# Optimization experiments

Hardware: AMD Instinct MI355X
Metric: run time of the kernel (lower is better)

Reference implementation:

```python
import jax, jax.numpy as jnp
import numpy as np

H = 32  # hidden size, fixed by the source module


def setup_inputs() -> dict:
    key = jax.random.key(0)
    ks = jax.random.split(key, 11)
    B, T = 1024, 999
    s = 0.1  # weight init scale
    return {
        "input": jax.random.normal(ks[0], (B, T), jnp.float32),
        "W_ih1": jax.random.normal(ks[1], (4 * H, 1), jnp.float32) * s,
        "W_hh1": jax.random.normal(ks[2], (4 * H, H), jnp.float32) * s,
        "b_ih1": jax.random.normal(ks[3], (4 * H,), jnp.float32) * s,
        "b_hh1": jax.random.normal(ks[4], (4 * H,), jnp.float32) * s,
        "W_ih2": jax.random.normal(ks[5], (4 * H, H), jnp.float32) * s,
        "W_hh2": jax.random.normal(ks[6], (4 * H, H), jnp.float32) * s,
        "b_ih2": jax.random.normal(ks[7], (4 * H,), jnp.float32) * s,
        "b_hh2": jax.random.normal(ks[8], (4 * H,), jnp.float32) * s,
        "W_lin": jax.random.normal(ks[9], (1, H), jnp.float32) * s,
        "b_lin": jax.random.normal(ks[10], (1,), jnp.float32) * s,
        "future": 1000,
    }


def _lstm_cell(x, h, c, W_ih, W_hh, b_ih, b_hh):
    # PyTorch LSTMCell: gates = x@W_ih^T + b_ih + h@W_hh^T + b_hh, order i,f,g,o
    z = x @ W_ih.T + h @ W_hh.T + (b_ih + b_hh)
    i, f, g, o = jnp.split(z, 4, axis=-1)
    c_new = jax.nn.sigmoid(f) * c + jax.nn.sigmoid(i) * jnp.tanh(g)
    h_new = jax.nn.sigmoid(o) * jnp.tanh(c_new)
    return h_new, c_new


def reference(input, W_ih1, W_hh1, b_ih1, b_hh1, W_ih2, W_hh2, b_ih2, b_hh2,
              W_lin, b_lin, future):
    B = input.shape[0]
    dt = input.dtype
    z = jnp.zeros((B, H), dt)

    def step_tf(carry, x_t):  # teacher-forced phase, x_t: [B]
        h1, c1, h2, c2 = carry
        h1, c1 = _lstm_cell(x_t[:, None], h1, c1, W_ih1, W_hh1, b_ih1, b_hh1)
        h2, c2 = _lstm_cell(h1, h2, c2, W_ih2, W_hh2, b_ih2, b_hh2)
        out = h2 @ W_lin.T + b_lin  # [B,1]
        return (h1, c1, h2, c2), out[:, 0]

    carry, outs1 = jax.lax.scan(step_tf, (z, z, z, z), input.T)  # outs1: [T,B]

    def step_gen(carry, _):
        h1, c1, h2, c2, out = carry
        h1, c1 = _lstm_cell(out, h1, c1, W_ih1, W_hh1, b_ih1, b_hh1)
        h2, c2 = _lstm_cell(h1, h2, c2, W_ih2, W_hh2, b_ih2, b_hh2)
        out = h2 @ W_lin.T + b_lin
        return (h1, c1, h2, c2, out), out[:, 0]

    last_out = outs1[-1][:, None]
    _, outs2 = jax.lax.scan(step_gen, (*carry, last_out), None, length=future)

    return jnp.concatenate([outs1, outs2], axis=0).T  # [B, T+future]
```

## Files before the change

### kernel.cpp

```cpp
#include <hip/hip_runtime.h>

#define HH 32
#define LOG2E 1.44269504088896340736f
#define KCH 16

typedef float v2f __attribute__((ext_vector_type(2)));

#define DPPF(v, ctrl) \
    __int_as_float(__builtin_amdgcn_update_dpp(0, __float_as_int(v), (ctrl), 0xF, 0xF, true))
#define QP_B0 0x00
#define QP_B1 0x55
#define QP_B2 0xAA
#define QP_B3 0xFF
#define DPP_ROR4  0x124
#define DPP_ROR8  0x128
#define SWZ(v, pat) __int_as_float(__builtin_amdgcn_ds_swizzle(__float_as_int(v), (pat)))

__device__ __forceinline__ float hw_exp2(float x) {
    float r; asm("v_exp_f32 %0, %1" : "=v"(r) : "v"(x)); return r;
}
__device__ __forceinline__ float sigm_e(float z, float e) {
    return __builtin_amdgcn_rcpf(1.0f + hw_exp2(z * e));
}
__device__ __forceinline__ v2f pk_fma(v2f a, v2f b, v2f c) {
    return __builtin_elementwise_fma(a, b, c);
}
__device__ __forceinline__ void load_bc(const float* p, v2f* d) {
#pragma unroll
    for (int r = 0; r < 8; ++r) {
        float4 v = ((const float4*)p)[r];
        d[2*r]   = (v2f){v.x, v.y};
        d[2*r+1] = (v2f){v.z, v.w};
    }
}
__device__ __forceinline__ float out_reduce(float p) {
    p += DPPF(p, DPP_ROR4);
    p += DPPF(p, DPP_ROR8);
    p += SWZ(p, 0x401F);
    p += __shfl_xor(p, 32, 64);
    return p;
}
__device__ __forceinline__ float rl(float v, int lane) {
    return __int_as_float(__builtin_amdgcn_readlane(__float_as_int(v), lane));
}
__device__ __forceinline__ float xo_reduce(float p) {
    p += DPPF(p, DPP_ROR4);
    p += DPPF(p, DPP_ROR8);
    float a0 = rl(p, 0), a1 = rl(p, 16), a2 = rl(p, 32), a3 = rl(p, 48);
    return (a0 + a1) + (a2 + a3);
}

template<bool ACC>
__device__ __forceinline__ void dot2(const v2f* hv, const v2f* mA, const v2f* mB,
                                     v2f& P0, v2f& P1, v2f& P2, v2f& P3) {
    if (ACC) {
        P0 = pk_fma(hv[0], mA[0], P0); P1 = pk_fma(hv[1], mA[1], P1);
        P2 = pk_fma(hv[0], mB[0], P2); P3 = pk_fma(hv[1], mB[1], P3);
    } else {
        P0 = hv[0] * mA[0]; P1 = hv[1] * mA[1];
        P2 = hv[0] * mB[0]; P3 = hv[1] * mB[1];
    }
#pragma unroll
    for (int r = 2; r < 16; r += 2) {
        P0 = pk_fma(hv[r],   mA[r],   P0);
        P1 = pk_fma(hv[r+1], mA[r+1], P1);
        P2 = pk_fma(hv[r],   mB[r],   P2);
        P3 = pk_fma(hv[r+1], mB[r+1], P3);
    }
}

__device__ __forceinline__ void gate_hc(float zA, float zB, float es, float mm, float cc,
                                        float& cA, float& cB, float& hA, float& hB) {
    float acA = fmaf(mm, sigm_e(zA, es), cc);
    float acB = fmaf(mm, sigm_e(zB, es), cc);
    float iA = DPPF(acA, QP_B0), fA = DPPF(acA, QP_B1);
    float gA = DPPF(acA, QP_B2), oA = DPPF(acA, QP_B3);
    float iB = DPPF(acB, QP_B0), fB = DPPF(acB, QP_B1);
    float gB = DPPF(acB, QP_B2), oB = DPPF(acB, QP_B3);
    cA = fmaf(fA, cA, iA * gA);
    cB = fmaf(fB, cB, iB * gB);
    hA = oA * fmaf(2.0f, sigm_e(cA, -2.0f * LOG2E), -1.0f);
    hB = oB * fmaf(2.0f, sigm_e(cB, -2.0f * LOG2E), -1.0f);
}

__global__ __launch_bounds__(128, 2)
void lstm_seq_kernel(const float* __restrict__ input,
                     const float* __restrict__ W_ih1, const float* __restrict__ W_hh1,
                     const float* __restrict__ b_ih1, const float* __restrict__ b_hh1,
                     const float* __restrict__ W_ih2, const float* __restrict__ W_hh2,
                     const float* __restrict__ b_ih2, const float* __restrict__ b_hh2,
                     const float* __restrict__ W_lin, const float* __restrict__ b_lin,
                     float* __restrict__ out, int T, int total)
{
    const int b    = blockIdx.x;
    const int tid  = threadIdx.x;
    const int w    = tid >> 6;
    const int lane = tid & 63;
    const int q    = lane & 3;
    const int ch   = lane >> 2;
    const int rowA = (q << 5) | ch;
    const int rowB = (q << 5) | (ch + 16);

    __shared__ __align__(16) float ring[2 * KCH * HH];
    __shared__ __align__(16) float h1x[HH];
    __shared__ __align__(16) float h2s[HH];
    __shared__ __align__(16) float c2x[HH];

    const bool  isg = (q == 2);
    const float es  = isg ? (-2.0f * LOG2E) : (-LOG2E);
    const float mm  = isg ? 2.0f : 1.0f;
    const float cc  = isg ? -1.0f : 0.0f;

    v2f m1A[16], m1B[16], m2A[16], m2B[16];
    float wxA = 0.f, wxB = 0.f, bA, bB, blin;
    const float wlA = W_lin[ch], wlB = W_lin[ch + 16];
    if (w == 0) {
        const v2f* pA = (const v2f*)(W_hh1 + rowA * HH);
        const v2f* pB = (const v2f*)(W_hh1 + rowB * HH);
#pragma unroll
        for (int r = 0; r < 16; ++r) { m1A[r] = pA[r]; m1B[r] = pB[r]; }
        wxA = W_ih1[rowA]; wxB = W_ih1[rowB];
        bA  = b_ih1[rowA] + b_hh1[rowA];
        bB  = b_ih1[rowB] + b_hh1[rowB];
    } else {
        const v2f* pA = (const v2f*)(W_ih2 + rowA * HH);
        const v2f* pB = (const v2f*)(W_ih2 + rowB * HH);
        const v2f* qA = (const v2f*)(W_hh2 + rowA * HH);
        const v2f* qB = (const v2f*)(W_hh2 + rowB * HH);
#pragma unroll
        for (int r = 0; r < 16; ++r) { m1A[r] = pA[r]; m1B[r] = pB[r];
                                       m2A[r] = qA[r]; m2B[r] = qB[r]; }
        bA  = b_ih2[rowA] + b_hh2[rowA];
        bB  = b_ih2[rowB] + b_hh2[rowB];
    }
    blin = b_lin[0];

    float cA = 0.f, cB = 0.f;
    v2f p0 = {0.f,0.f}, p1 = {0.f,0.f}, p2 = {0.f,0.f}, p3 = {0.f,0.f};

    const float* __restrict__ inp  = input + (size_t)b * T;
    float* __restrict__       outp = out   + (size_t)b * total;

    if (w == 0) {
        int t = 0;
        float xcur = inp[0];
        for (int cb = 0; t < T; ++cb) {
            float* buf = ring + (cb & 1) * (KCH * HH);
            int S = T - t; if (S > KCH) S = KCH;
            for (int s = 0; s < S; ++s, ++t) {
                float x = xcur;
                int tn = t + 1;
                xcur = inp[tn < T ? tn : 0];
                float z1A = fmaf(x, wxA, bA + (p0.x + p0.y) + (p1.x + p1.y));
                float z1B = fmaf(x, wxB, bB + (p2.x + p2.y) + (p3.x + p3.y));
                float hA, hB;
                gate_hc(z1A, z1B, es, mm, cc, cA, cB, hA, hB);
                float* slot = buf + s * HH;
                if (q == 0) { slot[ch] = hA; slot[ch + 16] = hB; }
                v2f hv[16]; load_bc(slot, hv);
                dot2<false>(hv, m1A, m1B, p0, p1, p2, p3);
            }
            __syncthreads();
        }
        __syncthreads();
    } else {
        __syncthreads();
        int t = 0;
        for (int cb = 0; t < T; ++cb) {
            const float* buf = ring + (cb & 1) * (KCH * HH);
            int S = T - t; if (S > KCH) S = KCH;
            for (int s = 0; s < S; ++s, ++t) {
                v2f hv[16]; load_bc(buf + s * HH, hv);
                dot2<true>(hv, m1A, m1B, p0, p1, p2, p3);
                float z2A = bA + (p0.x + p0.y) + (p1.x + p1.y);
                float z2B = bB + (p2.x + p2.y) + (p3.x + p3.y);
                float hA, hB;
                gate_hc(z2A, z2B, es, mm, cc, cA, cB, hA, hB);
                if (q == 0) { h2s[ch] = hA; h2s[ch + 16] = hB; }
                v2f gv[16]; load_bc(h2s, gv);
                dot2<false>(gv, m2A, m2B, p0, p1, p2, p3);
                float pr = fmaf(hA, wlA, hB * wlB);
                float ov = out_reduce(pr) + blin;
                if (lane == 0) outp[t] = ov;
            }
            if (t >= T && q == 0) { c2x[ch] = cA; c2x[ch + 16] = cB; }
            __syncthreads();
        }
        return;
    }

    float h2a = h2s[ch], h2b = h2s[ch + 16];
    float c2A = c2x[ch], c2B = c2x[ch + 16];
    v2f i2A[16], i2B[16], w2A[16], w2B[16];
    {
        const v2f* a1 = (const v2f*)(W_ih2 + rowA * HH);
        const v2f* a2 = (const v2f*)(W_ih2 + rowB * HH);
        const v2f* a3 = (const v2f*)(W_hh2 + rowA * HH);
        const v2f* a4 = (const v2f*)(W_hh2 + rowB * HH);
#pragma unroll
        for (int r = 0; r < 16; ++r) { i2A[r] = a1[r]; i2B[r] = a2[r];
                                       w2A[r] = a3[r]; w2B[r] = a4[r]; }
    }
    const float b2A = b_ih2[rowA] + b_hh2[rowA];
    const float b2B = b_ih2[rowB] + b_hh2[rowB];

    v2f tv[16]; load_bc(h2s, tv);

    for (int t = T; t < total; ++t) {
        float pr = fmaf(h2a, wlA, h2b * wlB);
        float xo = xo_reduce(pr) + blin;
        if (t > T && lane == 0) outp[t - 1] = xo;
        float z1A = fmaf(xo, wxA, bA + (p0.x + p0.y) + (p1.x + p1.y));
        float z1B = fmaf(xo, wxB, bB + (p2.x + p2.y) + (p3.x + p3.y));
        float hA, hB;
        gate_hc(z1A, z1B, es, mm, cc, cA, cB, hA, hB);
        v2f s0, s1, s2, s3;
        dot2<false>(tv, w2A, w2B, s0, s1, s2, s3);
        if (q == 0) { h1x[ch] = hA; h1x[ch + 16] = hB; }
        load_bc(h1x, tv);
        dot2<true>(tv, i2A, i2B, s0, s1, s2, s3);
        float z2A = b2A + (s0.x + s0.y) + (s1.x + s1.y);
        float z2B = b2B + (s2.x + s2.y) + (s3.x + s3.y);
        float h2n, h2m;
        gate_hc(z2A, z2B, es, mm, cc, c2A, c2B, h2n, h2m);
        h2a = h2n; h2b = h2m;
        dot2<false>(tv, m1A, m1B, p0, p1, p2, p3);
        if (q == 0) { h2s[ch] = h2a; h2s[ch + 16] = h2b; }
        load_bc(h2s, tv);
    }
    {
        float pr = fmaf(h2a, wlA, h2b * wlB);
        float ov = xo_reduce(pr) + blin;
        if (lane == 0) outp[total - 1] = ov;
    }
}

extern "C" void kernel_launch(void* const* d_in, const int* in_sizes, int n_in,
                              void* d_out, int out_size, void* d_ws, size_t ws_size,
                              hipStream_t stream) {
    const int B = 1024;
    const int T = in_sizes[0] / B;
    const int total = out_size / B;

    lstm_seq_kernel<<<dim3(B), dim3(128), 0, stream>>>(
        (const float*)d_in[0],
        (const float*)d_in[1], (const float*)d_in[2],
        (const float*)d_in[3], (const float*)d_in[4],
        (const float*)d_in[5], (const float*)d_in[6],
        (const float*)d_in[7], (const float*)d_in[8],
        (const float*)d_in[9], (const float*)d_in[10],
        (float*)d_out, T, total);
}
```

Baseline: 1.236 ms.

## Split LSTM work into a three-stage four-wave pipeline with smaller per-wave weights

```diff
diff --git a/kernel.cpp b/kernel.cpp
--- a/kernel.cpp
+++ b/kernel.cpp
@@ -24,6 +24,10 @@
 }
 __device__ __forceinline__ v2f pk_fma(v2f a, v2f b, v2f c) {
     return __builtin_elementwise_fma(a, b, c);
+}
+__device__ __forceinline__ void wave_barrier() {
+    asm volatile("s_waitcnt lgkmcnt(0)" ::: "memory");
+    __builtin_amdgcn_s_barrier();
 }
 __device__ __forceinline__ void load_bc(const float* p, v2f* d) {
 #pragma unroll
@@ -83,7 +87,7 @@
     hB = oB * fmaf(2.0f, sigm_e(cB, -2.0f * LOG2E), -1.0f);
 }
 
-__global__ __launch_bounds__(128, 2)
+__global__ __launch_bounds__(256, 4)
 void lstm_seq_kernel(const float* __restrict__ input,
                      const float* __restrict__ W_ih1, const float* __restrict__ W_hh1,
                      const float* __restrict__ b_ih1, const float* __restrict__ b_hh1,
@@ -94,16 +98,21 @@
 {
     const int b    = blockIdx.x;
     const int tid  = threadIdx.x;
-    const int w    = tid >> 6;
+    const int wv   = tid >> 6;
     const int lane = tid & 63;
     const int q    = lane & 3;
     const int ch   = lane >> 2;
     const int rowA = (q << 5) | ch;
     const int rowB = (q << 5) | (ch + 16);
-
-    __shared__ __align__(16) float ring[2 * KCH * HH];
+    const int zidx = (q << 4) | ch;
+
+    __shared__ __align__(16) float h1ring[2][KCH][HH];
+    __shared__ __align__(16) float zring[2][KCH][128];
     __shared__ __align__(16) float h1x[HH];
     __shared__ __align__(16) float h2s[HH];
+    __shared__ __align__(16) float zx0[128];
+    __shared__ __align__(16) float zx1[128];
+    __shared__ __align__(16) float zx2[128];
     __shared__ __align__(16) float c2x[HH];
 
     const bool  isg = (q == 2);
@@ -111,29 +120,21 @@
     const float mm  = isg ? 2.0f : 1.0f;
     const float cc  = isg ? -1.0f : 0.0f;
 
-    v2f m1A[16], m1B[16], m2A[16], m2B[16];
-    float wxA = 0.f, wxB = 0.f, bA, bB, blin;
+    v2f mA[16], mB[16];
+    {
+        const float* Wsel = (wv == 1) ? W_ih2 : (wv == 2) ? W_hh2 : W_hh1;
+        const v2f* pA = (const v2f*)(Wsel + rowA * HH);
+        const v2f* pB = (const v2f*)(Wsel + rowB * HH);
+#pragma unroll
+        for (int r = 0; r < 16; ++r) { mA[r] = pA[r]; mB[r] = pB[r]; }
+    }
+    const float wxA = W_ih1[rowA], wxB = W_ih1[rowB];
+    const float b1A = b_ih1[rowA] + b_hh1[rowA];
+    const float b1B = b_ih1[rowB] + b_hh1[rowB];
+    const float b2A = b_ih2[rowA] + b_hh2[rowA];
+    const float b2B = b_ih2[rowB] + b_hh2[rowB];
     const float wlA = W_lin[ch], wlB = W_lin[ch + 16];
-    if (w == 0) {
-        const v2f* pA = (const v2f*)(W_hh1 + rowA * HH);
-        const v2f* pB = (const v2f*)(W_hh1 + rowB * HH);
-#pragma unroll
-        for (int r = 0; r < 16; ++r) { m1A[r] = pA[r]; m1B[r] = pB[r]; }
-        wxA = W_ih1[rowA]; wxB = W_ih1[rowB];
-        bA  = b_ih1[rowA] + b_hh1[rowA];
-        bB  = b_ih1[rowB] + b_hh1[rowB];
-    } else {
-        const v2f* pA = (const v2f*)(W_ih2 + rowA * HH);
-        const v2f* pB = (const v2f*)(W_ih2 + rowB * HH);
-        const v2f* qA = (const v2f*)(W_hh2 + rowA * HH);
-        const v2f* qB = (const v2f*)(W_hh2 + rowB * HH);
-#pragma unroll
-        for (int r = 0; r < 16; ++r) { m1A[r] = pA[r]; m1B[r] = pB[r];
-                                       m2A[r] = qA[r]; m2B[r] = qB[r]; }
-        bA  = b_ih2[rowA] + b_hh2[rowA];
-        bB  = b_ih2[rowB] + b_hh2[rowB];
-    }
-    blin = b_lin[0];
+    const float blin = b_lin[0];
 
     float cA = 0.f, cB = 0.f;
     v2f p0 = {0.f,0.f}, p1 = {0.f,0.f}, p2 = {0.f,0.f}, p3 = {0.f,0.f};
@@ -141,95 +142,136 @@
     const float* __restrict__ inp  = input + (size_t)b * T;
     float* __restrict__       outp = out   + (size_t)b * total;
 
-    if (w == 0) {
-        int t = 0;
-        float xcur = inp[0];
-        for (int cb = 0; t < T; ++cb) {
-            float* buf = ring + (cb & 1) * (KCH * HH);
-            int S = T - t; if (S > KCH) S = KCH;
-            for (int s = 0; s < S; ++s, ++t) {
-                float x = xcur;
-                int tn = t + 1;
-                xcur = inp[tn < T ? tn : 0];
-                float z1A = fmaf(x, wxA, bA + (p0.x + p0.y) + (p1.x + p1.y));
-                float z1B = fmaf(x, wxB, bB + (p2.x + p2.y) + (p3.x + p3.y));
+    const int NCH = (T + KCH - 1) / KCH;
+    float xcur = (wv == 0) ? inp[0] : 0.f;
+    for (int k = 0; k <= NCH + 1; ++k) {
+        if (wv == 0) {
+            if (k < NCH) {
+                const int t0 = k * KCH;
+                int S = T - t0; if (S > KCH) S = KCH;
+                float* ring = &h1ring[k & 1][0][0];
+                for (int s = 0; s < S; ++s) {
+                    const int t = t0 + s;
+                    float x = xcur;
+                    int tn = t + 1;
+                    xcur = inp[tn < T ? tn : 0];
+                    v2f tA = p0 + p1, tB = p2 + p3;
+                    float z1A = fmaf(x, wxA, b1A + tA.x + tA.y);
+                    float z1B = fmaf(x, wxB, b1B + tB.x + tB.y);
+                    float hA, hB;
+                    gate_hc(z1A, z1B, es, mm, cc, cA, cB, hA, hB);
+                    float* slot = ring + s * HH;
+                    if (q == 0) {
+                        slot[ch] = hA; slot[ch + 16] = hB;
+                        if (t == T - 1) { h1x[ch] = hA; h1x[ch + 16] = hB; }
+                    }
+                    v2f hv[16]; load_bc(slot, hv);
+                    dot2<false>(hv, mA, mB, p0, p1, p2, p3);
+                }
+            }
+        } else if (wv == 1) {
+            if (k >= 1 && k <= NCH) {
+                const int c = k - 1, t0 = c * KCH;
+                int S = T - t0; if (S > KCH) S = KCH;
+                const float* ring = &h1ring[c & 1][0][0];
+                float* zb = &zring[c & 1][0][0];
+                for (int s = 0; s < S; ++s) {
+                    v2f hv[16]; load_bc(ring + s * HH, hv);
+                    v2f s0, s1, s2, s3;
+                    dot2<false>(hv, mA, mB, s0, s1, s2, s3);
+                    v2f uA = s0 + s1, uB = s2 + s3;
+                    float* zs = zb + s * 128;
+                    zs[zidx]      = uA.x + uA.y;
+                    zs[zidx + 64] = uB.x + uB.y;
+                }
+            }
+        } else if (wv == 2) {
+            if (k >= 2) {
+                const int c = k - 2, t0 = c * KCH;
+                int S = T - t0; if (S > KCH) S = KCH;
+                const float* zb = &zring[c & 1][0][0];
+                for (int s = 0; s < S; ++s) {
+                    const int t = t0 + s;
+                    const float* zs = zb + s * 128;
+                    float ziA = zs[zidx], ziB = zs[zidx + 64];
+                    v2f tA = p0 + p1, tB = p2 + p3;
+                    float z2A = b2A + ziA + tA.x + tA.y;
+                    float z2B = b2B + ziB + tB.x + tB.y;
+                    float hA, hB;
+                    gate_hc(z2A, z2B, es, mm, cc, cA, cB, hA, hB);
+                    if (q == 0) { h2s[ch] = hA; h2s[ch + 16] = hB; }
+                    v2f gv[16]; load_bc(h2s, gv);
+                    dot2<false>(gv, mA, mB, p0, p1, p2, p3);
+                    float pr = fmaf(hA, wlA, hB * wlB);
+                    float ov = out_reduce(pr) + blin;
+                    if (lane == 0) outp[t] = ov;
+                }
+                if (k == NCH + 1 && q == 0) { c2x[ch] = cA; c2x[ch + 16] = cB; }
+            }
+        }
+        wave_barrier();
+    }
+
+    v2f wl[16];
+    float h2a = 0.f, h2b = 0.f, d2A = 0.f, d2B = 0.f;
+    if (wv == 0) {
+        const v2f* wp = (const v2f*)W_lin;
+#pragma unroll
+        for (int r = 0; r < 16; ++r) wl[r] = wp[r];
+        h2a = h2s[ch]; h2b = h2s[ch + 16];
+        d2A = c2x[ch]; d2B = c2x[ch + 16];
+    }
+
+    for (int t = T; t < total; ++t) {
+        if (wv == 0) {
+            if (t > T) {
+                float z2A = b2A + zx1[zidx]      + zx2[zidx];
+                float z2B = b2B + zx1[zidx + 64] + zx2[zidx + 64];
                 float hA, hB;
-                gate_hc(z1A, z1B, es, mm, cc, cA, cB, hA, hB);
-                float* slot = buf + s * HH;
-                if (q == 0) { slot[ch] = hA; slot[ch + 16] = hB; }
-                v2f hv[16]; load_bc(slot, hv);
-                dot2<false>(hv, m1A, m1B, p0, p1, p2, p3);
-            }
-            __syncthreads();
+                gate_hc(z2A, z2B, es, mm, cc, d2A, d2B, hA, hB);
+                h2a = hA; h2b = hB;
+                if (q == 0) { h2s[ch] = h2a; h2s[ch + 16] = h2b; }
+            }
+            float pr = fmaf(h2a, wlA, h2b * wlB);
+            float xo = xo_reduce(pr) + blin;
+            if (t > T && lane == 0) outp[t - 1] = xo;
+            float zx0A, zx0B;
+            if (t == T) { v2f tA = p0 + p1, tB = p2 + p3; zx0A = tA.x + tA.y; zx0B = tB.x + tB.y; }
+            else        { zx0A = zx0[zidx]; zx0B = zx0[zidx + 64]; }
+            float z1A = fmaf(xo, wxA, b1A + zx0A);
+            float z1B = fmaf(xo, wxB, b1B + zx0B);
+            float hA, hB;
+            gate_hc(z1A, z1B, es, mm, cc, cA, cB, hA, hB);
+            if (q == 0) { h1x[ch] = hA; h1x[ch + 16] = hB; }
         }
-        __syncthreads();
-    } else {
-        __syncthreads();
-        int t = 0;
-        for (int cb = 0; t < T; ++cb) {
-            const float* buf = ring + (cb & 1) * (KCH * HH);
-            int S = T - t; if (S > KCH) S = KCH;
-            for (int s = 0; s < S; ++s, ++t) {
-                v2f hv[16]; load_bc(buf + s * HH, hv);
-                dot2<true>(hv, m1A, m1B, p0, p1, p2, p3);
-                float z2A = bA + (p0.x + p0.y) + (p1.x + p1.y);
-                float z2B = bB + (p2.x + p2.y) + (p3.x + p3.y);
-                float hA, hB;
-                gate_hc(z2A, z2B, es, mm, cc, cA, cB, hA, hB);
-                if (q == 0) { h2s[ch] = hA; h2s[ch + 16] = hB; }
-                v2f gv[16]; load_bc(h2s, gv);
-                dot2<false>(gv, m2A, m2B, p0, p1, p2, p3);
-                float pr = fmaf(hA, wlA, hB * wlB);
-                float ov = out_reduce(pr) + blin;
-                if (lane == 0) outp[t] = ov;
-            }
-            if (t >= T && q == 0) { c2x[ch] = cA; c2x[ch + 16] = cB; }
-            __syncthreads();
+        wave_barrier();
+        if (wv == 1) {
+            v2f hv[16]; load_bc(h1x, hv);
+            v2f s0, s1, s2, s3;
+            dot2<false>(hv, mA, mB, s0, s1, s2, s3);
+            v2f uA = s0 + s1, uB = s2 + s3;
+            zx1[zidx] = uA.x + uA.y; zx1[zidx + 64] = uB.x + uB.y;
+        } else if (wv == 3) {
+            v2f hv[16]; load_bc(h1x, hv);
+            v2f s0, s1, s2, s3;
+            dot2<false>(hv, mA, mB, s0, s1, s2, s3);
+            v2f uA = s0 + s1, uB = s2 + s3;
+            zx0[zidx] = uA.x + uA.y; zx0[zidx + 64] = uB.x + uB.y;
+        } else if (wv == 2) {
+            v2f gv[16]; load_bc(h2s, gv);
+            v2f s0, s1, s2, s3;
+            dot2<false>(gv, mA, mB, s0, s1, s2, s3);
+            v2f uA = s0 + s1, uB = s2 + s3;
+            zx2[zidx] = uA.x + uA.y; zx2[zidx + 64] = uB.x + uB.y;
         }
-        return;
-    }
-
-    float h2a = h2s[ch], h2b = h2s[ch + 16];
-    float c2A = c2x[ch], c2B = c2x[ch + 16];
-    v2f i2A[16], i2B[16], w2A[16], w2B[16];
-    {
-        const v2f* a1 = (const v2f*)(W_ih2 + rowA * HH);
-        const v2f* a2 = (const v2f*)(W_ih2 + rowB * HH);
-        const v2f* a3 = (const v2f*)(W_hh2 + rowA * HH);
-        const v2f* a4 = (const v2f*)(W_hh2 + rowB * HH);
-#pragma unroll
-        for (int r = 0; r < 16; ++r) { i2A[r] = a1[r]; i2B[r] = a2[r];
-                                       w2A[r] = a3[r]; w2B[r] = a4[r]; }
-    }
-    const float b2A = b_ih2[rowA] + b_hh2[rowA];
-    const float b2B = b_ih2[rowB] + b_hh2[rowB];
-
-    v2f tv[16]; load_bc(h2s, tv);
-
-    for (int t = T; t < total; ++t) {
-        float pr = fmaf(h2a, wlA, h2b * wlB);
-        float xo = xo_reduce(pr) + blin;
-        if (t > T && lane == 0) outp[t - 1] = xo;
-        float z1A = fmaf(xo, wxA, bA + (p0.x + p0.y) + (p1.x + p1.y));
-        float z1B = fmaf(xo, wxB, bB + (p2.x + p2.y) + (p3.x + p3.y));
+        wave_barrier();
+    }
+    if (wv == 0) {
+        float z2A = b2A + zx1[zidx]      + zx2[zidx];
+        float z2B = b2B + zx1[zidx + 64] + zx2[zidx + 64];
         float hA, hB;
-        gate_hc(z1A, z1B, es, mm, cc, cA, cB, hA, hB);
-        v2f s0, s1, s2, s3;
-        dot2<false>(tv, w2A, w2B, s0, s1, s2, s3);
-        if (q == 0) { h1x[ch] = hA; h1x[ch + 16] = hB; }
-        load_bc(h1x, tv);
-        dot2<true>(tv, i2A, i2B, s0, s1, s2, s3);
-        float z2A = b2A + (s0.x + s0.y) + (s1.x + s1.y);
-        float z2B = b2B + (s2.x + s2.y) + (s3.x + s3.y);
-        float h2n, h2m;
-        gate_hc(z2A, z2B, es, mm, cc, c2A, c2B, h2n, h2m);
-        h2a = h2n; h2b = h2m;
-        dot2<false>(tv, m1A, m1B, p0, p1, p2, p3);
-        if (q == 0) { h2s[ch] = h2a; h2s[ch + 16] = h2b; }
-        load_bc(h2s, tv);
-    }
-    {
-        float pr = fmaf(h2a, wlA, h2b * wlB);
+        gate_hc(z2A, z2B, es, mm, cc, d2A, d2B, hA, hB);
+        float pr = fmaf(hA, wlA, hB * wlB);
         float ov = xo_reduce(pr) + blin;
         if (lane == 0) outp[total - 1] = ov;
     }
@@ -242,7 +284,7 @@
     const int T = in_sizes[0] / B;
     const int total = out_size / B;
 
-    lstm_seq_kernel<<<dim3(B), dim3(128), 0, stream>>>(
+    lstm_seq_kernel<<<dim3(B), dim3(256), 0, stream>>>(
         (const float*)d_in[0],
         (const float*)d_in[1], (const float*)d_in[2],
         (const float*)d_in[3], (const float*)d_in[4],
```

Measured after the change: 1.418 ms. +14.7%, slower.
